# Performance work log

Measured on AMD Instinct MI355X. Metric: run time of the kernel, lower is better.

The kernel has to match this reference:

```python
import jax, jax.numpy as jnp
import numpy as np

B, L, D, H, FF = 32, 577, 512, 8, 2048  # L = sequence_length + 1
DK = D // H
EPS = 1e-6


def setup_inputs() -> dict:
    key = jax.random.key(0)
    ks = jax.random.split(key, 16)
    s = lambda fan_in: 1.0 / np.sqrt(fan_in)
    inp = {
        "x": jax.random.normal(ks[0], (B, L, D), dtype=jnp.float32),
        # whole-sequence LayerNorm params (flattened over L*D)
        "gamma1": jnp.ones((L * D,), jnp.float32),
        "beta1": jnp.zeros((L * D,), jnp.float32),
        "gamma2": jnp.ones((L * D,), jnp.float32),
        "beta2": jnp.zeros((L * D,), jnp.float32),
        # attention projections, stored [in, out] (torch Linear weight transposed)
        "wq": jax.random.uniform(ks[1], (D, D), jnp.float32, -s(D), s(D)),
        "bq": jax.random.uniform(ks[2], (D,), jnp.float32, -s(D), s(D)),
        "wk": jax.random.uniform(ks[3], (D, D), jnp.float32, -s(D), s(D)),
        "bk": jax.random.uniform(ks[4], (D,), jnp.float32, -s(D), s(D)),
        "wv": jax.random.uniform(ks[5], (D, D), jnp.float32, -s(D), s(D)),
        "bv": jax.random.uniform(ks[6], (D,), jnp.float32, -s(D), s(D)),
        "wo": jax.random.uniform(ks[7], (D, D), jnp.float32, -s(D), s(D)),
        "bo": jax.random.uniform(ks[8], (D,), jnp.float32, -s(D), s(D)),
        # FFN 512 -> 2048 -> 512
        "w1": jax.random.uniform(ks[9], (D, FF), jnp.float32, -s(D), s(D)),
        "b1": jax.random.uniform(ks[10], (FF,), jnp.float32, -s(D), s(D)),
        "w2": jax.random.uniform(ks[11], (FF, D), jnp.float32, -s(FF), s(FF)),
        "b2": jax.random.uniform(ks[12], (D,), jnp.float32, -s(FF), s(FF)),
    }
    return inp


def _whole_seq_layernorm(x, gamma, beta):
    # Flattens [B, L, D] -> [B, L*D]; stats over all tokens jointly.
    xf = x.reshape(x.shape[0], -1)
    mean = jnp.mean(xf, axis=-1, keepdims=True)
    std = jnp.std(xf, axis=-1, keepdims=True, ddof=1)  # torch .std() is unbiased
    out = gamma * ((xf - mean) / (std + EPS)) + beta
    return out.reshape(x.shape)


def _mha(x, wq, bq, wk, bk, wv, bv, wo, bo):
    q = (x @ wq + bq).reshape(B, L, H, DK)
    k = (x @ wk + bk).reshape(B, L, H, DK)
    v = (x @ wv + bv).reshape(B, L, H, DK)
    # NOTE: original scales by 1/sqrt(d_model), not 1/sqrt(d_k)
    scores = jnp.einsum("blhd,bmhd->bhlm", q, k) / jnp.sqrt(jnp.float32(D))
    w = jax.nn.softmax(scores, axis=-1)
    o = jnp.einsum("bhlm,bmhd->blhd", w, v).reshape(B, L, D)
    return o @ wo + bo


def reference(x, gamma1, beta1, gamma2, beta2, wq, bq, wk, bk, wv, bv, wo, bo, w1, b1, w2, b2):
    h = _whole_seq_layernorm(x, gamma1, beta1)
    h = _mha(h, wq, bq, wk, bk, wv, bv, wo, bo) + x
    g = _whole_seq_layernorm(h, gamma2, beta2)
    ff = jax.nn.gelu(g @ w1 + b1, approximate=False) @ w2 + b2
    return ff + h
```

## Files before the change

kernel.cpp:

```cpp
#include <hip/hip_runtime.h>
#include <math.h>

typedef unsigned short u16;
typedef __attribute__((ext_vector_type(8))) short short8;
typedef __attribute__((ext_vector_type(4))) float f32x4;
typedef __attribute__((ext_vector_type(16))) float f32x16;

constexpr int NB = 32, NL = 577, ND = 512, NH = 8, NDK = 64, NFF = 2048;
constexpr int NTOK = NB * NL;
constexpr int NLP  = 640;
constexpr int LDN  = NL * ND;
constexpr size_t QKVE = (size_t)NB * NH * NLP * NDK;

__device__ __forceinline__ u16 f2bf(float f) {
  union { float f; unsigned u; } v; v.f = f;
  unsigned r = v.u + 0x7fffu + ((v.u >> 16) & 1u);
  return (u16)(r >> 16);
}
__device__ __forceinline__ void gload_lds16(const void* g, void* l) {
  __builtin_amdgcn_global_load_lds((const __attribute__((address_space(1))) void*)g,
                                   (__attribute__((address_space(3))) void*)l, 16, 0, 0);
}
__device__ __forceinline__ int xcd_swz(int lin, int nwg) {
  const int xcd = lin & 7, o = lin >> 3;
  const int q = nwg >> 3, r = nwg & 7;
  return (xcd < r ? xcd * (q + 1) : r * (q + 1) + (xcd - r) * q) + o;
}
__device__ __forceinline__ unsigned cvt_pk_bf16(float a, float b) {
  unsigned r;
  asm("v_cvt_pk_bf16_f32 %0, %1, %2" : "=v"(r) : "v"(a), "v"(b));
  return r;
}
__device__ __forceinline__ float exp2_f(float x) {
  float r;
  asm("v_exp_f32 %0, %1" : "=v"(r) : "v"(x));
  return r;
}
__device__ __forceinline__ short8 mk8(unsigned a, unsigned b, unsigned c, unsigned d) {
  union { unsigned u[4]; short8 v; } f;
  f.u[0] = a; f.u[1] = b; f.u[2] = c; f.u[3] = d;
  return f.v;
}
__device__ __forceinline__ f32x16 mfma32(short8 a, short8 b, f32x16 c) {
  return __builtin_amdgcn_mfma_f32_32x32x16_bf16(a, b, c, 0, 0, 0);
}
__device__ __forceinline__ f32x4 mfma16(short8 a, short8 b, f32x4 c) {
  return __builtin_amdgcn_mfma_f32_16x16x32_bf16(a, b, c, 0, 0, 0);
}

__global__ void pad_zero(u16* __restrict__ qb, u16* __restrict__ kb, u16* __restrict__ vt,
                         float* __restrict__ stats,
                         const float* __restrict__ bq, const float* __restrict__ bk,
                         const float* __restrict__ bv, float* __restrict__ cbias) {
  const int i = blockIdx.x * 256 + threadIdx.x;
  if (i < 128) stats[i] = 0.f;
  if (i < 1536) cbias[i] = i < 512 ? bq[i] : (i < 1024 ? bk[i - 512] : bv[i - 1024]);
  const int NPQ = 256 * 63 * 64;
  if (i < NPQ) {
    const int bh = i / (63 * 64), rem = i - bh * (63 * 64);
    const int r = rem >> 6, d = rem & 63;
    const size_t o = ((size_t)bh * NLP + 577 + r) * NDK + d;
    qb[o] = 0; kb[o] = 0;
    const int d2 = rem / 63, kv = rem - d2 * 63;
    vt[((size_t)bh * NDK + d2) * NLP + 577 + kv] = 0;
  }
}

__global__ void ln_stats(const float* __restrict__ x, float* __restrict__ stats) {
  const int b = blockIdx.x, s = blockIdx.y;
  const int per4 = LDN / 8 / 4;
  const float4* xb = (const float4*)(x + (size_t)b * LDN + (size_t)s * (LDN / 8));
  float sum = 0.f, ss = 0.f;
  for (int i = threadIdx.x; i < per4; i += blockDim.x) {
    float4 v = xb[i];
    sum += v.x + v.y + v.z + v.w;
    ss  += v.x * v.x + v.y * v.y + v.z * v.z + v.w * v.w;
  }
#pragma unroll
  for (int o = 32; o; o >>= 1) { sum += __shfl_down(sum, o); ss += __shfl_down(ss, o); }
  __shared__ float s0[4], s1[4];
  const int lane = threadIdx.x & 63, w = threadIdx.x >> 6;
  if (lane == 0) { s0[w] = sum; s1[w] = ss; }
  __syncthreads();
  if (threadIdx.x == 0) {
    atomicAdd(&stats[b * 2 + 0], s0[0] + s0[1] + s0[2] + s0[3]);
    atomicAdd(&stats[b * 2 + 1], s1[0] + s1[1] + s1[2] + s1[3]);
  }
}

__global__ void ln_apply(const float* __restrict__ x, const float* __restrict__ stats,
                         const float* __restrict__ gamma, const float* __restrict__ beta,
                         u16* __restrict__ out) {
  const int nv = LDN / 4;
  const size_t total = (size_t)NB * nv;
  for (size_t i = (size_t)blockIdx.x * blockDim.x + threadIdx.x; i < total;
       i += (size_t)gridDim.x * blockDim.x) {
    const int b = (int)(i / nv);
    const int j = (int)(i - (size_t)b * nv);
    const float sum = stats[b * 2], ssum = stats[b * 2 + 1];
    const float mean = sum / (float)LDN;
    const float var = (ssum - (float)LDN * mean * mean) / (float)(LDN - 1);
    const float inv = 1.0f / (sqrtf(var) + 1e-6f);
    const float4 xv = ((const float4*)x)[i];
    const float4 gv = ((const float4*)gamma)[j];
    const float4 bv = ((const float4*)beta)[j];
    ushort4 o;
    o.x = f2bf(gv.x * ((xv.x - mean) * inv) + bv.x);
    o.y = f2bf(gv.y * ((xv.y - mean) * inv) + bv.y);
    o.z = f2bf(gv.z * ((xv.z - mean) * inv) + bv.z);
    o.w = f2bf(gv.w * ((xv.w - mean) * inv) + bv.w);
    ((ushort4*)out)[i] = o;
  }
}

__global__ void transpose_bf16(const float* __restrict__ w, u16* __restrict__ wt,
                               int K, int N) {
  const size_t total = (size_t)K * N;
  for (size_t i = (size_t)blockIdx.x * blockDim.x + threadIdx.x; i < total;
       i += (size_t)gridDim.x * blockDim.x) {
    const int k = (int)(i / N), n = (int)(i - (size_t)k * N);
    wt[(size_t)n * K + k] = f2bf(w[i]);
  }
}
__global__ void transpose_qkv(const float* __restrict__ wq, const float* __restrict__ wk,
                              const float* __restrict__ wv, u16* __restrict__ wt) {
  const size_t total = (size_t)1536 * 512;
  for (size_t i = (size_t)blockIdx.x * blockDim.x + threadIdx.x; i < total;
       i += (size_t)gridDim.x * blockDim.x) {
    const int n = (int)(i >> 9), k = (int)(i & 511);
    const int s = n >> 9, c = n & 511;
    const float* src = s == 0 ? wq : (s == 1 ? wk : wv);
    wt[i] = f2bf(src[(size_t)k * 512 + c]);
  }
}

template <int EPI>
__global__ __launch_bounds__(256, 4) void gemm_bt(
    const u16* __restrict__ A, const u16* __restrict__ Bt,
    int M, int N, int K, int lda, int ldb,
    const float* __restrict__ bias,
    const float* __restrict__ res, int ldr,
    void* __restrict__ outp, float oscale, float* __restrict__ stats) {
  __shared__ __align__(16) u16 lA[128 * 64];
  __shared__ __align__(16) u16 lB[128 * 64];
  int lin = blockIdx.x + blockIdx.y * gridDim.x;
  lin = xcd_swz(lin, gridDim.x * gridDim.y);
  const int bx = lin / gridDim.y, by = lin - (lin / gridDim.y) * gridDim.y;
  const int m0 = bx * 128, n0 = by * 128;
  const int tid = threadIdx.x, lane = tid & 63, wid = tid >> 6;
  const int l16 = lane & 15, l4 = lane >> 4;
  const int wm = wid >> 1, wn = wid & 1;

  f32x4 acc[4][4] = {};

  for (int k0 = 0; k0 < K; k0 += 64) {
#pragma unroll
    for (int j = 0; j < 4; j++) {
      const int cb = j * 256 + wid * 64;
      const int c = cb + lane;
      const int row = c >> 3, g = c & 7;
      const int scol = k0 + ((g ^ (row & 7)) << 3);
      gload_lds16(A + (size_t)(m0 + row) * lda + scol, &lA[cb * 8]);
      gload_lds16(Bt + (size_t)(n0 + row) * ldb + scol, &lB[cb * 8]);
    }
    __syncthreads();
#pragma unroll
    for (int ks = 0; ks < 2; ks++) {
      short8 af[4], bfr[4];
#pragma unroll
      for (int mi = 0; mi < 4; mi++) {
        const int rl = wm * 64 + mi * 16 + l16;
        af[mi] = *(const short8*)&lA[rl * 64 + (((ks * 4 + l4) ^ (rl & 7)) << 3)];
      }
#pragma unroll
      for (int ni = 0; ni < 4; ni++) {
        const int rl = wn * 64 + ni * 16 + l16;
        bfr[ni] = *(const short8*)&lB[rl * 64 + (((ks * 4 + l4) ^ (rl & 7)) << 3)];
      }
#pragma unroll
      for (int mi = 0; mi < 4; mi++)
#pragma unroll
        for (int ni = 0; ni < 4; ni++)
          acc[mi][ni] = mfma16(af[mi], bfr[ni], acc[mi][ni]);
    }
    __syncthreads();
  }

  float sm0 = 0.f, sm1 = 0.f, sq0 = 0.f, sq1 = 0.f;
#pragma unroll
  for (int mi = 0; mi < 4; mi++) {
#pragma unroll
    for (int r = 0; r < 4; r++) {
      const int row = m0 + wm * 64 + mi * 16 + l4 * 4 + r;
      if (row >= M) continue;
      int rb = 0, rl = 0, which = 0;
      if (EPI == 0) { rb = row / NL; rl = row - rb * NL; }
      if (EPI == 6) which = (row >= (m0 / NL + 1) * NL) ? 1 : 0;
#pragma unroll
      for (int ni = 0; ni < 4; ni++) {
        const int col = n0 + wn * 64 + ni * 16 + l16;
        if (col >= N) continue;
        const float v = acc[mi][ni][r];
        if (EPI == 0) {
          const int kind = col >> 9, c = col & 511, h = c >> 6, d = c & 63;
          const float val = v + bias[col];
          u16* base = (u16*)outp;
          if (kind == 0)
            base[(((size_t)rb * NH + h) * NLP + rl) * NDK + d] = f2bf(val * oscale);
          else if (kind == 1)
            (base + QKVE)[(((size_t)rb * NH + h) * NLP + rl) * NDK + d] = f2bf(val);
          else
            (base + 2 * QKVE)[(((size_t)rb * NH + h) * NDK + d) * NLP + rl] = f2bf(val);
        } else if (EPI == 4 || EPI == 6) {
          const float hv = v + bias[col] + res[(size_t)row * ldr + col];
          ((float*)outp)[(size_t)row * N + col] = hv;
          if (EPI == 6) {
            if (which) { sm1 += hv; sq1 += hv * hv; }
            else       { sm0 += hv; sq0 += hv * hv; }
          }
        } else {
          const float t = v + bias[col];
          const float u = 0.7978845608028654f * t * (1.0f + 0.044715f * t * t);
          const float e = __expf(-2.0f * fabsf(u));
          float th = (1.0f - e) * __builtin_amdgcn_rcpf(1.0f + e);
          th = u < 0.f ? -th : th;
          ((u16*)outp)[(size_t)row * N + col] = f2bf(0.5f * t * (1.0f + th));
        }
      }
    }
  }
  if (EPI == 6) {
#pragma unroll
    for (int o = 32; o; o >>= 1) {
      sm0 += __shfl_down(sm0, o); sq0 += __shfl_down(sq0, o);
      sm1 += __shfl_down(sm1, o); sq1 += __shfl_down(sq1, o);
    }
    if (lane == 0) {
      const int b0 = m0 / NL;
      atomicAdd(&stats[b0 * 2 + 0], sm0);
      atomicAdd(&stats[b0 * 2 + 1], sq0);
      if (b0 + 1 < NB) {
        atomicAdd(&stats[(b0 + 1) * 2 + 0], sm1);
        atomicAdd(&stats[(b0 + 1) * 2 + 1], sq1);
      }
    }
  }
}

__global__ __launch_bounds__(64, 2) void attn_fused(
    const u16* __restrict__ qb, const u16* __restrict__ kb,
    const u16* __restrict__ vt, u16* __restrict__ aog) {
  const int lane = threadIdx.x & 63;
  const int l32 = lane & 31, hi = lane >> 5;
  int lin = blockIdx.x + blockIdx.y * gridDim.x;
  lin = xcd_swz(lin, gridDim.x * gridDim.y);
  const int qt = lin % 10, bh = lin / 10;
  const int q0 = qt * 64;
  const u16* QpA = qb + (size_t)bh * NLP * NDK + (size_t)(q0 + l32) * NDK + hi * 8;
  const u16* Kp = kb + (size_t)bh * NLP * NDK + (size_t)l32 * NDK + hi * 8;
  const u16* Vp = vt + (size_t)bh * NDK * NLP + (size_t)l32 * NLP + hi * 8;

  short8 qfA[4], qfB[4];
#pragma unroll
  for (int kc = 0; kc < 4; kc++) {
    qfA[kc] = *(const short8*)(QpA + kc * 16);
    qfB[kc] = *(const short8*)(QpA + (size_t)32 * NDK + kc * 16);
  }

  f32x16 oA0 = {}, oA1 = {}, oB0 = {}, oB1 = {};
  float mA = -3e38f, lA = 0.f, mB = -3e38f, lB = 0.f;

  for (int kv0 = 0; kv0 < NLP; kv0 += 64) {
    short8 ka[4], kh[4];
#pragma unroll
    for (int kc = 0; kc < 4; kc++) {
      ka[kc] = *(const short8*)(Kp + (size_t)kv0 * NDK + kc * 16);
      kh[kc] = *(const short8*)(Kp + (size_t)(kv0 + 32) * NDK + kc * 16);
    }
    f32x16 sA0 = {}, sA1 = {}, sB0 = {}, sB1 = {};
    __builtin_amdgcn_s_setprio(1);
#pragma unroll
    for (int kc = 0; kc < 4; kc++) {
      sA0 = mfma32(ka[kc], qfA[kc], sA0);
      sA1 = mfma32(kh[kc], qfA[kc], sA1);
      sB0 = mfma32(ka[kc], qfB[kc], sB0);
      sB1 = mfma32(kh[kc], qfB[kc], sB1);
    }
    __builtin_amdgcn_s_setprio(0);
    short8 vf0[4], vf1[4];
#pragma unroll
    for (int ks = 0; ks < 4; ks++) {
      vf0[ks] = *(const short8*)(Vp + (size_t)(kv0 + ks * 16));
      vf1[ks] = *(const short8*)(Vp + (size_t)32 * NLP + (kv0 + ks * 16));
    }
    if (kv0 + 64 > NL) {
#pragma unroll
      for (int r = 0; r < 16; r++) {
        const int kvb = kv0 + (r & 3) + 8 * (r >> 2) + 4 * hi;
        const bool v0 = kvb < NL, v1 = kvb + 32 < NL;
        sA0[r] = v0 ? sA0[r] : -1e30f;
        sA1[r] = v1 ? sA1[r] : -1e30f;
        sB0[r] = v0 ? sB0[r] : -1e30f;
        sB1[r] = v1 ? sB1[r] : -1e30f;
      }
    }
#pragma unroll
    for (int half = 0; half < 2; half++) {
      f32x16& s0 = half ? sB0 : sA0;
      f32x16& s1 = half ? sB1 : sA1;
      f32x16& o0 = half ? oB0 : oA0;
      f32x16& o1 = half ? oB1 : oA1;
      float& m = half ? mB : mA;
      float& l = half ? lB : lA;
      float t4[8];
#pragma unroll
      for (int i = 0; i < 8; i++)
        t4[i] = fmaxf(fmaxf(s0[2 * i], s0[2 * i + 1]), fmaxf(s1[2 * i], s1[2 * i + 1]));
      float t = fmaxf(fmaxf(fmaxf(t4[0], t4[1]), fmaxf(t4[2], t4[3])),
                      fmaxf(fmaxf(t4[4], t4[5]), fmaxf(t4[6], t4[7])));
      t = fmaxf(t, __shfl_xor(t, 32));
      if (!__all(t - m <= 8.0f)) {
        const float mn = fmaxf(m, t);
        const float sc = exp2_f(m - mn);
        m = mn;
        l *= sc;
#pragma unroll
        for (int r = 0; r < 16; r++) { o0[r] *= sc; o1[r] *= sc; }
      }
      float rs = 0.f;
#pragma unroll
      for (int r = 0; r < 16; r++) { s0[r] = exp2_f(s0[r] - m); rs += s0[r]; }
#pragma unroll
      for (int r = 0; r < 16; r++) { s1[r] = exp2_f(s1[r] - m); rs += s1[r]; }
      l += rs + __shfl_xor(rs, 32);

      unsigned w0[8], w1[8], p0[8], p1[8];
#pragma unroll
      for (int i = 0; i < 8; i++) {
        w0[i] = cvt_pk_bf16(s0[2 * i], s0[2 * i + 1]);
        w1[i] = cvt_pk_bf16(s1[2 * i], s1[2 * i + 1]);
      }
#pragma unroll
      for (int i = 0; i < 8; i++) {
        p0[i] = (unsigned)__shfl_xor((int)w0[i], 32);
        p1[i] = (unsigned)__shfl_xor((int)w1[i], 32);
      }
      short8 pa[4];
      pa[0] = mk8(hi ? p0[2] : w0[0], hi ? p0[3] : w0[1], hi ? w0[2] : p0[0], hi ? w0[3] : p0[1]);
      pa[1] = mk8(hi ? p0[6] : w0[4], hi ? p0[7] : w0[5], hi ? w0[6] : p0[4], hi ? w0[7] : p0[5]);
      pa[2] = mk8(hi ? p1[2] : w1[0], hi ? p1[3] : w1[1], hi ? w1[2] : p1[0], hi ? w1[3] : p1[1]);
      pa[3] = mk8(hi ? p1[6] : w1[4], hi ? p1[7] : w1[5], hi ? w1[6] : p1[4], hi ? w1[7] : p1[5]);
      __builtin_amdgcn_s_setprio(1);
#pragma unroll
      for (int ks = 0; ks < 4; ks++) {
        o0 = mfma32(vf0[ks], pa[ks], o0);
        o1 = mfma32(vf1[ks], pa[ks], o1);
      }
      __builtin_amdgcn_s_setprio(0);
    }
  }

  const int b = bh >> 3, h = bh & 7;
#pragma unroll
  for (int half = 0; half < 2; half++) {
    const int qg = q0 + half * 32 + l32;
    if (qg >= NL) continue;
    const f32x16& o0 = half ? oB0 : oA0;
    const f32x16& o1 = half ? oB1 : oA1;
    const float inv = 1.0f / (half ? lB : lA);
    u16* orow = aog + ((size_t)b * NL + qg) * ND + h * NDK;
#pragma unroll
    for (int r = 0; r < 16; r += 2) {
      const int d = (r & 3) + 4 * hi + 8 * (r >> 2);
      *(unsigned*)(orow + d) = cvt_pk_bf16(o0[r] * inv, o0[r + 1] * inv);
      *(unsigned*)(orow + 32 + d) = cvt_pk_bf16(o1[r] * inv, o1[r + 1] * inv);
    }
  }
}

extern "C" void kernel_launch(void* const* d_in, const int* in_sizes, int n_in,
                              void* d_out, int out_size, void* d_ws, size_t ws_size,
                              hipStream_t stream) {
  const float* x      = (const float*)d_in[0];
  const float* gamma1 = (const float*)d_in[1];
  const float* beta1  = (const float*)d_in[2];
  const float* gamma2 = (const float*)d_in[3];
  const float* beta2  = (const float*)d_in[4];
  const float* wq = (const float*)d_in[5];
  const float* bq = (const float*)d_in[6];
  const float* wk = (const float*)d_in[7];
  const float* bk = (const float*)d_in[8];
  const float* wv = (const float*)d_in[9];
  const float* bv = (const float*)d_in[10];
  const float* wo = (const float*)d_in[11];
  const float* bo = (const float*)d_in[12];
  const float* w1 = (const float*)d_in[13];
  const float* b1 = (const float*)d_in[14];
  const float* w2 = (const float*)d_in[15];
  const float* b2 = (const float*)d_in[16];
  float* out = (float*)d_out;

  char* ws = (char*)d_ws;
  size_t off = 0;
  auto take = [&](size_t bytes) { size_t o = off; off += (bytes + 255) & ~(size_t)255; return o; };
  const size_t SLK = 2u << 20;

  float* stats = (float*)(ws + take(512));
  float* stats1 = stats;
  float* stats2 = stats + 64;
  float* cbias = (float*)(ws + take(1536 * 4));
  u16* wqkvT = (u16*)(ws + take((size_t)1536 * 512 * 2));
  u16* woT = (u16*)(ws + take((size_t)512 * 512 * 2));
  u16* w1T = (u16*)(ws + take((size_t)512 * 2048 * 2));
  u16* w2T = (u16*)(ws + take((size_t)2048 * 512 * 2));
  float* hbuf = (float*)(ws + take((size_t)NTOK * ND * 4 + SLK));
  u16* qb = (u16*)(ws + take(3 * QKVE * 2 + SLK));
  u16* kb = qb + QKVE;
  u16* vt = kb + QKVE;
  u16* aog = (u16*)(ws + take((size_t)NTOK * ND * 2 + SLK));
  size_t r7 = take((size_t)NTOK * NFF * 2 + SLK);
  u16* xn   = (u16*)(ws + r7);
  u16* ubuf = (u16*)(ws + r7);

  pad_zero<<<(256 * 63 * 64 + 255) / 256, 256, 0, stream>>>(qb, kb, vt, stats, bq, bk, bv, cbias);

  transpose_qkv<<<1536, 256, 0, stream>>>(wq, wk, wv, wqkvT);
  transpose_bf16<<<512, 256, 0, stream>>>(wo, woT, 512, 512);
  transpose_bf16<<<2048, 256, 0, stream>>>(w1, w1T, 512, 2048);
  transpose_bf16<<<2048, 256, 0, stream>>>(w2, w2T, 2048, 512);

  ln_stats<<<dim3(NB, 8), 256, 0, stream>>>(x, stats1);
  ln_apply<<<2048, 256, 0, stream>>>(x, stats1, gamma1, beta1, xn);

  constexpr float QSCALE = 0.04419417382415922f * 1.4426950408889634f;
  gemm_bt<0><<<dim3(145, 12), 256, 0, stream>>>(xn, wqkvT, NTOK, 1536, ND, ND, ND,
                                                cbias, nullptr, 0, qb, QSCALE, nullptr);

  attn_fused<<<dim3(10, NB * NH), 64, 0, stream>>>(qb, kb, vt, aog);

  gemm_bt<6><<<dim3(145, 4), 256, 0, stream>>>(aog, woT, NTOK, ND, ND, ND, ND,
                                               bo, x, ND, hbuf, 1.0f, stats2);

  ln_apply<<<2048, 256, 0, stream>>>(hbuf, stats2, gamma2, beta2, aog);

  gemm_bt<5><<<dim3(145, 16), 256, 0, stream>>>(aog, w1T, NTOK, NFF, ND, ND, ND,
                                                b1, nullptr, 0, ubuf, 1.0f, nullptr);
  gemm_bt<4><<<dim3(145, 4), 256, 0, stream>>>(ubuf, w2T, NTOK, ND, NFF, NFF, NFF,
                                               b2, hbuf, ND, out, 1.0f, nullptr);
}
```

Before: 443.6 us.

## Add double-buffered 128x64 GEMM for N=512 projections and store residual in bf16

Adds a new gemm64 kernel with a 128x64 tile and double-buffered LDS staging, used for the output projection and FFN down-projection. This doubles the grid to 1160 blocks so the CUs are better filled, and it overlaps global loads with MFMA work. The intermediate residual h is now stored as bf16 instead of fp32, which halves its write and read traffic. A matching bf16-input LayerNorm kernel is added. The cost is lower precision in the residual stream, which adds error to the final output.

```diff
diff --git a/kernel.cpp b/kernel.cpp
--- a/kernel.cpp
+++ b/kernel.cpp
@@ -16,6 +16,9 @@
   union { float f; unsigned u; } v; v.f = f;
   unsigned r = v.u + 0x7fffu + ((v.u >> 16) & 1u);
   return (u16)(r >> 16);
+}
+__device__ __forceinline__ float bf2f(u16 h) {
+  union { unsigned u; float f; } v; v.u = ((unsigned)h) << 16; return v.f;
 }
 __device__ __forceinline__ void gload_lds16(const void* g, void* l) {
   __builtin_amdgcn_global_load_lds((const __attribute__((address_space(1))) void*)g,
@@ -113,6 +116,31 @@
   }
 }
 
+__global__ void ln_apply_b(const u16* __restrict__ x, const float* __restrict__ stats,
+                           const float* __restrict__ gamma, const float* __restrict__ beta,
+                           u16* __restrict__ out) {
+  const int nv = LDN / 4;
+  const size_t total = (size_t)NB * nv;
+  for (size_t i = (size_t)blockIdx.x * blockDim.x + threadIdx.x; i < total;
+       i += (size_t)gridDim.x * blockDim.x) {
+    const int b = (int)(i / nv);
+    const int j = (int)(i - (size_t)b * nv);
+    const float sum = stats[b * 2], ssum = stats[b * 2 + 1];
+    const float mean = sum / (float)LDN;
+    const float var = (ssum - (float)LDN * mean * mean) / (float)(LDN - 1);
+    const float inv = 1.0f / (sqrtf(var) + 1e-6f);
+    const ushort4 xv = ((const ushort4*)x)[i];
+    const float4 gv = ((const float4*)gamma)[j];
+    const float4 bv = ((const float4*)beta)[j];
+    ushort4 o;
+    o.x = f2bf(gv.x * ((bf2f(xv.x) - mean) * inv) + bv.x);
+    o.y = f2bf(gv.y * ((bf2f(xv.y) - mean) * inv) + bv.y);
+    o.z = f2bf(gv.z * ((bf2f(xv.z) - mean) * inv) + bv.z);
+    o.w = f2bf(gv.w * ((bf2f(xv.w) - mean) * inv) + bv.w);
+    ((ushort4*)out)[i] = o;
+  }
+}
+
 __global__ void transpose_bf16(const float* __restrict__ w, u16* __restrict__ wt,
                                int K, int N) {
   const size_t total = (size_t)K * N;
@@ -139,8 +167,7 @@
     const u16* __restrict__ A, const u16* __restrict__ Bt,
     int M, int N, int K, int lda, int ldb,
     const float* __restrict__ bias,
-    const float* __restrict__ res, int ldr,
-    void* __restrict__ outp, float oscale, float* __restrict__ stats) {
+    void* __restrict__ outp, float oscale) {
   __shared__ __align__(16) u16 lA[128 * 64];
   __shared__ __align__(16) u16 lB[128 * 64];
   int lin = blockIdx.x + blockIdx.y * gridDim.x;
@@ -186,16 +213,14 @@
     __syncthreads();
   }
 
-  float sm0 = 0.f, sm1 = 0.f, sq0 = 0.f, sq1 = 0.f;
 #pragma unroll
   for (int mi = 0; mi < 4; mi++) {
 #pragma unroll
     for (int r = 0; r < 4; r++) {
       const int row = m0 + wm * 64 + mi * 16 + l4 * 4 + r;
       if (row >= M) continue;
-      int rb = 0, rl = 0, which = 0;
+      int rb = 0, rl = 0;
       if (EPI == 0) { rb = row / NL; rl = row - rb * NL; }
-      if (EPI == 6) which = (row >= (m0 / NL + 1) * NL) ? 1 : 0;
 #pragma unroll
       for (int ni = 0; ni < 4; ni++) {
         const int col = n0 + wn * 64 + ni * 16 + l16;
@@ -211,13 +236,6 @@
             (base + QKVE)[(((size_t)rb * NH + h) * NLP + rl) * NDK + d] = f2bf(val);
           else
             (base + 2 * QKVE)[(((size_t)rb * NH + h) * NDK + d) * NLP + rl] = f2bf(val);
-        } else if (EPI == 4 || EPI == 6) {
-          const float hv = v + bias[col] + res[(size_t)row * ldr + col];
-          ((float*)outp)[(size_t)row * N + col] = hv;
-          if (EPI == 6) {
-            if (which) { sm1 += hv; sq1 += hv * hv; }
-            else       { sm0 += hv; sq0 += hv * hv; }
-          }
         } else {
           const float t = v + bias[col];
           const float u = 0.7978845608028654f * t * (1.0f + 0.044715f * t * t);
@@ -225,6 +243,100 @@
           float th = (1.0f - e) * __builtin_amdgcn_rcpf(1.0f + e);
           th = u < 0.f ? -th : th;
           ((u16*)outp)[(size_t)row * N + col] = f2bf(0.5f * t * (1.0f + th));
+        }
+      }
+    }
+  }
+}
+
+template <int EPI>
+__global__ __launch_bounds__(256, 3) void gemm64(
+    const u16* __restrict__ A, const u16* __restrict__ Bt,
+    int M, int N, int K, int lda, int ldb,
+    const float* __restrict__ bias,
+    const void* __restrict__ res, int ldr,
+    void* __restrict__ outp, float* __restrict__ stats) {
+  __shared__ __align__(16) u16 L[24576];
+  int lin = blockIdx.x + blockIdx.y * gridDim.x;
+  lin = xcd_swz(lin, gridDim.x * gridDim.y);
+  const int bx = lin / gridDim.y, by = lin - (lin / gridDim.y) * gridDim.y;
+  const int m0 = bx * 128, n0 = by * 64;
+  const int tid = threadIdx.x, lane = tid & 63, wid = tid >> 6;
+  const int l16 = lane & 15, l4 = lane >> 4;
+  const int wm = wid >> 1, wn = wid & 1;
+
+  f32x4 acc[4][2] = {};
+
+  auto stage = [&](int buf, int k0) {
+#pragma unroll
+    for (int j = 0; j < 4; j++) {
+      const int cb = j * 256 + wid * 64;
+      const int c = cb + lane;
+      const int row = c >> 3, g = c & 7;
+      gload_lds16(A + (size_t)(m0 + row) * lda + k0 + ((g ^ (row & 7)) << 3),
+                  &L[buf * 8192 + cb * 8]);
+    }
+#pragma unroll
+    for (int j = 0; j < 2; j++) {
+      const int cb = j * 256 + wid * 64;
+      const int c = cb + lane;
+      const int row = c >> 3, g = c & 7;
+      gload_lds16(Bt + (size_t)(n0 + row) * ldb + k0 + ((g ^ (row & 7)) << 3),
+                  &L[16384 + buf * 4096 + cb * 8]);
+    }
+  };
+
+  const int T = K >> 6;
+  stage(0, 0);
+  __syncthreads();
+  int cur = 0;
+  for (int t = 0; t < T; ++t) {
+    if (t + 1 < T) stage(cur ^ 1, (t + 1) << 6);
+    const int ao = cur * 8192, bo = 16384 + cur * 4096;
+#pragma unroll
+    for (int ks = 0; ks < 2; ks++) {
+      short8 af[4], bfr[2];
+#pragma unroll
+      for (int mi = 0; mi < 4; mi++) {
+        const int rl = wm * 64 + mi * 16 + l16;
+        af[mi] = *(const short8*)&L[ao + rl * 64 + (((ks * 4 + l4) ^ (rl & 7)) << 3)];
+      }
+#pragma unroll
+      for (int ni = 0; ni < 2; ni++) {
+        const int rl = wn * 32 + ni * 16 + l16;
+        bfr[ni] = *(const short8*)&L[bo + rl * 64 + (((ks * 4 + l4) ^ (rl & 7)) << 3)];
+      }
+#pragma unroll
+      for (int mi = 0; mi < 4; mi++)
+#pragma unroll
+        for (int ni = 0; ni < 2; ni++)
+          acc[mi][ni] = mfma16(af[mi], bfr[ni], acc[mi][ni]);
+    }
+    __syncthreads();
+    cur ^= 1;
+  }
+
+  float sm0 = 0.f, sm1 = 0.f, sq0 = 0.f, sq1 = 0.f;
+#pragma unroll
+  for (int mi = 0; mi < 4; mi++) {
+#pragma unroll
+    for (int r = 0; r < 4; r++) {
+      const int row = m0 + wm * 64 + mi * 16 + l4 * 4 + r;
+      if (row >= M) continue;
+      int which = 0;
+      if (EPI == 6) which = (row >= (m0 / NL + 1) * NL) ? 1 : 0;
+#pragma unroll
+      for (int ni = 0; ni < 2; ni++) {
+        const int col = n0 + wn * 32 + ni * 16 + l16;
+        const float v = acc[mi][ni][r];
+        if (EPI == 6) {
+          const float hv = v + bias[col] + ((const float*)res)[(size_t)row * ldr + col];
+          ((u16*)outp)[(size_t)row * N + col] = f2bf(hv);
+          if (which) { sm1 += hv; sq1 += hv * hv; }
+          else       { sm0 += hv; sq0 += hv * hv; }
+        } else {
+          ((float*)outp)[(size_t)row * N + col] =
+              v + bias[col] + bf2f(((const u16*)res)[(size_t)row * ldr + col]);
         }
       }
     }
@@ -413,7 +525,7 @@
   u16* woT = (u16*)(ws + take((size_t)512 * 512 * 2));
   u16* w1T = (u16*)(ws + take((size_t)512 * 2048 * 2));
   u16* w2T = (u16*)(ws + take((size_t)2048 * 512 * 2));
-  float* hbuf = (float*)(ws + take((size_t)NTOK * ND * 4 + SLK));
+  u16* hbuf = (u16*)(ws + take((size_t)NTOK * ND * 2 + SLK));
   u16* qb = (u16*)(ws + take(3 * QKVE * 2 + SLK));
   u16* kb = qb + QKVE;
   u16* vt = kb + QKVE;
@@ -434,17 +546,17 @@
 
   constexpr float QSCALE = 0.04419417382415922f * 1.4426950408889634f;
   gemm_bt<0><<<dim3(145, 12), 256, 0, stream>>>(xn, wqkvT, NTOK, 1536, ND, ND, ND,
-                                                cbias, nullptr, 0, qb, QSCALE, nullptr);
+                                                cbias, qb, QSCALE);
 
   attn_fused<<<dim3(10, NB * NH), 64, 0, stream>>>(qb, kb, vt, aog);
 
-  gemm_bt<6><<<dim3(145, 4), 256, 0, stream>>>(aog, woT, NTOK, ND, ND, ND, ND,
-                                               bo, x, ND, hbuf, 1.0f, stats2);
-
-  ln_apply<<<2048, 256, 0, stream>>>(hbuf, stats2, gamma2, beta2, aog);
+  gemm64<6><<<dim3(145, 8), 256, 0, stream>>>(aog, woT, NTOK, ND, ND, ND, ND,
+                                              bo, x, ND, hbuf, stats2);
+
+  ln_apply_b<<<2048, 256, 0, stream>>>(hbuf, stats2, gamma2, beta2, aog);
 
   gemm_bt<5><<<dim3(145, 16), 256, 0, stream>>>(aog, w1T, NTOK, NFF, ND, ND, ND,
-                                                b1, nullptr, 0, ubuf, 1.0f, nullptr);
-  gemm_bt<4><<<dim3(145, 4), 256, 0, stream>>>(ubuf, w2T, NTOK, ND, NFF, NFF, NFF,
-                                               b2, hbuf, ND, out, 1.0f, nullptr);
-}
+                                                b1, ubuf, 1.0f);
+  gemm64<4><<<dim3(145, 8), 256, 0, stream>>>(ubuf, w2T, NTOK, ND, NFF, NFF, NFF,
+                                              b2, hbuf, ND, out, nullptr);
+}
```

After: 506.2 us. +14.1%, slower.
